# Performance work log

Hardware: AMD Instinct MI355X
Metric: run time of the kernel (lower is better)

The kernel has to match this reference:

```python
import jax, jax.numpy as jnp
import numpy as np

D_IN = 3072      # == d_out (code reshapes x directly into heads)
D_OUT = 3072
N_HEADS = 16
HEAD_DIM = D_OUT // N_HEADS          # 192
D_C = D_OUT // 3                     # 1024, compressed latent dim
LN_EPS = 1e-5


def setup_inputs() -> dict:
    key = jax.random.key(0)
    ks = jax.random.split(key, 8)
    s = 0.02
    return {
        "x": jax.random.normal(ks[0], (2, 2048, D_IN), dtype=jnp.float32),
        "W_query": jax.random.normal(ks[1], (D_OUT, D_IN), dtype=jnp.float32) * s,
        "W_kv": jax.random.normal(ks[2], (D_C, D_IN), dtype=jnp.float32) * s,
        "W_uk": jax.random.normal(ks[3], (D_OUT, D_C), dtype=jnp.float32) * s,
        "W_uv": jax.random.normal(ks[4], (D_OUT, D_C), dtype=jnp.float32) * s,
        "W_out": jax.random.normal(ks[5], (D_OUT, D_OUT), dtype=jnp.float32) * s,
        "b_out": jnp.zeros((D_OUT,), dtype=jnp.float32),
        "ln_g": jnp.ones((D_C,), dtype=jnp.float32),
        "ln_b": jnp.zeros((D_C,), dtype=jnp.float32),
    }


def reference(x, W_query, W_kv, W_uk, W_uv, W_out, b_out, ln_g, ln_b):
    B, T, D = x.shape
    past_length = 0  # prefill, kv_cache=None

    # absorbed K projection: (d_out, d_in) @ (d_out, d_c) -> (H, head_dim, d_c)
    absorbed_k = (W_query @ W_uk).reshape(N_HEADS, HEAD_DIM, D_C)

    # compressed latent c_kv = LayerNorm(x @ W_kv^T), shape (B, S, d_c)
    c = x @ W_kv.T
    mu = jnp.mean(c, axis=-1, keepdims=True)
    var = jnp.mean(jnp.square(c - mu), axis=-1, keepdims=True)
    c_kv = (c - mu) * jax.lax.rsqrt(var + LN_EPS) * ln_g + ln_b
    S = c_kv.shape[1]

    # values decompressed: (B, S, H, head_dim)
    v = (c_kv @ W_uv.T).reshape(B, S, N_HEADS, HEAD_DIM)

    # queries: raw x reshaped into heads (as in the original code)
    q = x.reshape(B, T, N_HEADS, HEAD_DIM)

    # scores in compressed space: q @ absorbed_k @ c_kv^T
    tmp = jnp.einsum("bthd,hdc->bhtc", q, absorbed_k)           # (B,H,T,d_c)
    scores = jnp.einsum("bhtc,bsc->bhts", tmp, c_kv)
    scores = scores / np.float32(np.sqrt(HEAD_DIM))

    # causal mask with past_length offset (tril diagonal=past_length)
    row = jnp.arange(T)[:, None]
    col = jnp.arange(S)[None, :]
    mask = col <= (row + past_length)                            # (T,S) bool
    scores = jnp.where(mask[None, None], scores, -jnp.inf)

    weights = jax.nn.softmax(scores, axis=-1)                    # (B,H,T,S)

    ctx = jnp.einsum("bhts,bshd->bthd", weights, v).reshape(B, T, D_OUT)
    out = ctx @ W_out.T + b_out
    return out, c_kv
```

## Files before the change

### kernel.cpp

```cpp
#include <hip/hip_runtime.h>
#include <hip/hip_bf16.h>
#include <math.h>

#define BB 2
#define TT 2048
#define DD 3072
#define NH 16
#define HD 192
#define DC 1024

typedef __attribute__((ext_vector_type(8))) short bh8;
typedef __attribute__((ext_vector_type(4))) float f32x4;
typedef unsigned int u32;

__device__ __forceinline__ short f2b(float f) {
  __hip_bfloat16 h = __float2bfloat16(f);
  return *reinterpret_cast<short*>(&h);
}

__device__ __forceinline__ void gload16(const void* g, void* lds) {
  __builtin_amdgcn_global_load_lds(
      (const __attribute__((address_space(1))) u32*)g,
      (__attribute__((address_space(3))) u32*)lds, 16, 0, 0);
}

__global__ __launch_bounds__(256) void cast_f2b_k(const float* __restrict__ in,
                                                  short* __restrict__ out) {
  size_t i = ((size_t)blockIdx.x * 256 + threadIdx.x) * 8;
  float4 v0 = *(const float4*)&in[i];
  float4 v1 = *(const float4*)&in[i + 4];
  bh8 o;
  o[0] = f2b(v0.x); o[1] = f2b(v0.y); o[2] = f2b(v0.z); o[3] = f2b(v0.w);
  o[4] = f2b(v1.x); o[5] = f2b(v1.y); o[6] = f2b(v1.z); o[7] = f2b(v1.w);
  *(bh8*)&out[i] = o;
}

__global__ __launch_bounds__(256) void castT_f2b_k(const float* __restrict__ in,
                                                   short* __restrict__ out,
                                                   int R, int C) {
  __shared__ float t[64][65];
  const int cx = blockIdx.x * 64, ry = blockIdx.y * 64;
  const int tid = threadIdx.x, lx = tid & 15, ly = tid >> 4;
#pragma unroll
  for (int i = 0; i < 4; ++i) {
    int r = ly + i * 16;
    float4 v = *(const float4*)&in[(size_t)(ry + r) * C + cx + lx * 4];
    t[r][lx * 4 + 0] = v.x; t[r][lx * 4 + 1] = v.y;
    t[r][lx * 4 + 2] = v.z; t[r][lx * 4 + 3] = v.w;
  }
  __syncthreads();
#pragma unroll
  for (int i = 0; i < 4; ++i) {
    int c = ly + i * 16;
    ushort4 v;
    v.x = (unsigned short)f2b(t[lx * 4 + 0][c]);
    v.y = (unsigned short)f2b(t[lx * 4 + 1][c]);
    v.z = (unsigned short)f2b(t[lx * 4 + 2][c]);
    v.w = (unsigned short)f2b(t[lx * 4 + 3][c]);
    *(ushort4*)&out[(size_t)(cx + c) * R + ry + lx * 4] = v;
  }
}

__global__ __launch_bounds__(256) void transpose_b16_k(
    const unsigned short* __restrict__ in, unsigned short* __restrict__ out) {
  __shared__ unsigned short t[64][65];
  const unsigned short* ib = in + (size_t)blockIdx.z * TT * DD;
  unsigned short* ob = out + (size_t)blockIdx.z * DD * TT;
  const int cx = blockIdx.x * 64, ry = blockIdx.y * 64;
  const int tid = threadIdx.x, lx = tid & 15, ly = tid >> 4;
#pragma unroll
  for (int i = 0; i < 4; ++i) {
    int r = ly + i * 16;
    ushort4 v = *(const ushort4*)&ib[(size_t)(ry + r) * DD + cx + lx * 4];
    t[r][lx * 4 + 0] = v.x; t[r][lx * 4 + 1] = v.y;
    t[r][lx * 4 + 2] = v.z; t[r][lx * 4 + 3] = v.w;
  }
  __syncthreads();
#pragma unroll
  for (int i = 0; i < 4; ++i) {
    int c = ly + i * 16;
    ushort4 v;
    v.x = t[lx * 4 + 0][c]; v.y = t[lx * 4 + 1][c];
    v.z = t[lx * 4 + 2][c]; v.w = t[lx * 4 + 3][c];
    *(ushort4*)&ob[(size_t)(cx + c) * TT + ry + lx * 4] = v;
  }
}

template <bool OUTBF, bool BIAS>
__global__ __launch_bounds__(256) void gemm_bf16(
    const short* __restrict__ A, const short* __restrict__ Bt,
    const float* __restrict__ bias, void* __restrict__ Cout,
    int M, int N, int K) {
  __shared__ short As[4096];
  __shared__ short Bs[4096];
  const int tid = threadIdx.x;
  const int w = tid >> 6, l = tid & 63, lm = l & 15, lg = l >> 4;
  const int wr = w >> 1, wc = w & 1;
  const int m0 = blockIdx.y * 128, n0 = blockIdx.x * 128;

  f32x4 acc[4][4] = {};

  for (int k0 = 0; k0 < K; k0 += 32) {
    __syncthreads();
#pragma unroll
    for (int c = 0; c < 2; ++c) {
      int p = c * 256 + w * 64 + l;
      int row = p >> 2, kc = p & 3;
      int g = kc ^ ((row >> 1) & 3);
      gload16(&A[(size_t)(m0 + row) * K + k0 + g * 8],
              &As[(c * 256 + w * 64) * 8]);
      gload16(&Bt[(size_t)(n0 + row) * K + k0 + g * 8],
              &Bs[(c * 256 + w * 64) * 8]);
    }
    __syncthreads();

    bh8 a[4], b[4];
#pragma unroll
    for (int mi = 0; mi < 4; ++mi) {
      int r = wr * 64 + mi * 16 + lm;
      a[mi] = *(const bh8*)&As[r * 32 + ((lg ^ ((r >> 1) & 3)) << 3)];
    }
#pragma unroll
    for (int ni = 0; ni < 4; ++ni) {
      int r = wc * 64 + ni * 16 + lm;
      b[ni] = *(const bh8*)&Bs[r * 32 + ((lg ^ ((r >> 1) & 3)) << 3)];
    }
#pragma unroll
    for (int mi = 0; mi < 4; ++mi)
#pragma unroll
      for (int ni = 0; ni < 4; ++ni)
        acc[mi][ni] = __builtin_amdgcn_mfma_f32_16x16x32_bf16(
            a[mi], b[ni], acc[mi][ni], 0, 0, 0);
  }

#pragma unroll
  for (int mi = 0; mi < 4; ++mi) {
#pragma unroll
    for (int ni = 0; ni < 4; ++ni) {
      int row = m0 + wr * 64 + mi * 16 + lg * 4;
      int col = n0 + wc * 64 + ni * 16 + lm;
      float bi = 0.f;
      if (BIAS) bi = bias[col];
#pragma unroll
      for (int r = 0; r < 4; ++r) {
        float v = acc[mi][ni][r] + bi;
        if (OUTBF)
          ((short*)Cout)[(size_t)(row + r) * N + col] = f2b(v);
        else
          ((float*)Cout)[(size_t)(row + r) * N + col] = v;
      }
    }
  }
}

__global__ __launch_bounds__(256) void ln_k(const float* __restrict__ cpre,
                                            const float* __restrict__ g,
                                            const float* __restrict__ bta,
                                            float* __restrict__ o32,
                                            short* __restrict__ o16) {
  const int row = blockIdx.x;
  const int tid = threadIdx.x;
  __shared__ float red1[4];
  __shared__ float red2[4];

  float4 v = *(const float4*)&cpre[(size_t)row * DC + tid * 4];
  float s = v.x + v.y + v.z + v.w;
#pragma unroll
  for (int mk = 32; mk; mk >>= 1) s += __shfl_xor(s, mk, 64);
  if ((tid & 63) == 0) red1[tid >> 6] = s;
  __syncthreads();
  float mu = (red1[0] + red1[1] + red1[2] + red1[3]) * (1.f / DC);

  float dx = v.x - mu, dy = v.y - mu, dz = v.z - mu, dw = v.w - mu;
  float s2 = dx * dx + dy * dy + dz * dz + dw * dw;
#pragma unroll
  for (int mk = 32; mk; mk >>= 1) s2 += __shfl_xor(s2, mk, 64);
  if ((tid & 63) == 0) red2[tid >> 6] = s2;
  __syncthreads();
  float var = (red2[0] + red2[1] + red2[2] + red2[3]) * (1.f / DC);
  float rs = rsqrtf(var + 1e-5f);

  float4 gg = *(const float4*)&g[tid * 4];
  float4 bb = *(const float4*)&bta[tid * 4];
  float4 o;
  o.x = dx * rs * gg.x + bb.x;
  o.y = dy * rs * gg.y + bb.y;
  o.z = dz * rs * gg.z + bb.z;
  o.w = dw * rs * gg.w + bb.w;
  *(float4*)&o32[(size_t)row * DC + tid * 4] = o;
  ushort4 ob;
  ob.x = (unsigned short)f2b(o.x); ob.y = (unsigned short)f2b(o.y);
  ob.z = (unsigned short)f2b(o.z); ob.w = (unsigned short)f2b(o.w);
  *(ushort4*)&o16[(size_t)row * DC + tid * 4] = ob;
}

__global__ __launch_bounds__(256) void attn_mfma(
    const short* __restrict__ xb, const short* __restrict__ kfull,
    const short* __restrict__ vT, short* __restrict__ ctx) {
  __shared__ short Ks[64 * 192];
  __shared__ short Vs[192 * 64];
  __shared__ short Ps[4][16 * 64];

  const int idx = blockIdx.x;
  const int qt = 31 - (idx >> 5);
  const int bh = idx & 31;
  const int h = bh & 15, b = bh >> 4;
  const int tid = threadIdx.x, w = tid >> 6, l = tid & 63;
  const int lm = l & 15, lg = l >> 4;
  const int qw0 = qt * 64 + w * 16;
  const float QS = 0.07216878364870323f;

  bh8 qf[6];
  {
    const short* qrow = &xb[(size_t)(b * TT + qw0 + lm) * DD + h * HD];
#pragma unroll
    for (int kq = 0; kq < 6; ++kq)
      qf[kq] = *(const bh8*)&qrow[kq * 32 + lg * 8];
  }

  f32x4 o[12] = {};
  float mrun[4], lrun[4];
#pragma unroll
  for (int r = 0; r < 4; ++r) { mrun[r] = -INFINITY; lrun[r] = 0.f; }

  for (int st = 0; st <= qt; ++st) {
    const int s0 = st * 64;
    __syncthreads();
#pragma unroll
    for (int c = 0; c < 6; ++c) {
      int p = c * 256 + w * 64 + l;
      {
        int krow = p / 24, kc = p - krow * 24;
        int g = kc ^ (krow & 7);
        gload16(&kfull[(size_t)(b * TT + s0 + krow) * DD + h * HD + g * 8],
                &Ks[(c * 256 + w * 64) * 8]);
      }
      {
        int vrow = p >> 3, vc = p & 7;
        int gv = vc ^ (vrow & 7);
        gload16(&vT[(size_t)((b * NH + h) * HD + vrow) * TT + s0 + gv * 8],
                &Vs[(c * 256 + w * 64) * 8]);
      }
    }
    __syncthreads();

    f32x4 s[4] = {};
    __builtin_amdgcn_s_setprio(1);
#pragma unroll
    for (int nf = 0; nf < 4; ++nf) {
      const int krow = nf * 16 + lm;
      const short* kr = &Ks[krow * 192];
#pragma unroll
      for (int kq = 0; kq < 6; ++kq) {
        bh8 kb = *(const bh8*)&kr[(((kq * 4 + lg) ^ (krow & 7)) << 3)];
        s[nf] = __builtin_amdgcn_mfma_f32_16x16x32_bf16(qf[kq], kb, s[nf],
                                                        0, 0, 0);
      }
    }
    __builtin_amdgcn_s_setprio(0);

    float pv[4][4];
#pragma unroll
    for (int nf = 0; nf < 4; ++nf)
#pragma unroll
      for (int r = 0; r < 4; ++r) pv[nf][r] = s[nf][r] * QS;
    if (st == qt) {
#pragma unroll
      for (int nf = 0; nf < 4; ++nf)
#pragma unroll
        for (int r = 0; r < 4; ++r)
          if (nf * 16 + lm > w * 16 + lg * 4 + r) pv[nf][r] = -INFINITY;
    }
#pragma unroll
    for (int r = 0; r < 4; ++r) {
      float mt = fmaxf(fmaxf(pv[0][r], pv[1][r]), fmaxf(pv[2][r], pv[3][r]));
#pragma unroll
      for (int mk = 1; mk < 16; mk <<= 1) mt = fmaxf(mt, __shfl_xor(mt, mk));
      float mnew = fmaxf(mrun[r], mt);
      float corr = __expf(mrun[r] - mnew);
      mrun[r] = mnew;
      float ls = 0.f;
#pragma unroll
      for (int nf = 0; nf < 4; ++nf) {
        float p = __expf(pv[nf][r] - mnew);
        pv[nf][r] = p;
        ls += p;
      }
#pragma unroll
      for (int mk = 1; mk < 16; mk <<= 1) ls += __shfl_xor(ls, mk);
      lrun[r] = lrun[r] * corr + ls;
#pragma unroll
      for (int nf = 0; nf < 12; ++nf) o[nf][r] *= corr;
    }
#pragma unroll
    for (int nf = 0; nf < 4; ++nf)
#pragma unroll
      for (int r = 0; r < 4; ++r) {
        int prow = lg * 4 + r;
        int col = nf * 16 + lm;
        int sc = (((col >> 3) ^ (prow & 7)) << 3) + (col & 7);
        Ps[w][prow * 64 + sc] = f2b(pv[nf][r]);
      }

    bh8 pa0, pa1;
    {
      int prow = lm;
      pa0 = *(const bh8*)&Ps[w][prow * 64 + ((lg ^ (prow & 7)) << 3)];
      pa1 = *(const bh8*)&Ps[w][prow * 64 + (((4 + lg) ^ (prow & 7)) << 3)];
    }
    __builtin_amdgcn_s_setprio(1);
#pragma unroll
    for (int nf = 0; nf < 12; ++nf) {
      int drow = nf * 16 + lm;
      const short* vr = &Vs[drow * 64];
      bh8 vb0 = *(const bh8*)&vr[((lg ^ (drow & 7)) << 3)];
      bh8 vb1 = *(const bh8*)&vr[(((4 + lg) ^ (drow & 7)) << 3)];
      o[nf] = __builtin_amdgcn_mfma_f32_16x16x32_bf16(pa0, vb0, o[nf], 0, 0, 0);
      o[nf] = __builtin_amdgcn_mfma_f32_16x16x32_bf16(pa1, vb1, o[nf], 0, 0, 0);
    }
    __builtin_amdgcn_s_setprio(0);
  }

#pragma unroll
  for (int r = 0; r < 4; ++r) {
    float inv = 1.f / lrun[r];
    int row = qw0 + lg * 4 + r;
    short* cp = &ctx[(size_t)(b * TT + row) * DD + h * HD];
#pragma unroll
    for (int nf = 0; nf < 12; ++nf)
      cp[nf * 16 + lm] = f2b(o[nf][r] * inv);
  }
}

extern "C" void kernel_launch(void* const* d_in, const int* in_sizes, int n_in,
                              void* d_out, int out_size, void* d_ws,
                              size_t ws_size, hipStream_t stream) {
  const float* x    = (const float*)d_in[0];
  const float* Wq   = (const float*)d_in[1];
  const float* Wkv  = (const float*)d_in[2];
  const float* Wuk  = (const float*)d_in[3];
  const float* Wuv  = (const float*)d_in[4];
  const float* Wout = (const float*)d_in[5];
  const float* bout = (const float*)d_in[6];
  const float* lng  = (const float*)d_in[7];
  const float* lnb  = (const float*)d_in[8];

  float* out   = (float*)d_out;
  float* ckv32 = out + (size_t)BB * TT * DD;

  char* W = (char*)d_ws;
  short* xb     = (short*)(W);
  short* wbuf   = (short*)(W + 25165824);
  short* wukT   = (short*)(W + 44040192);
  short* wkvb   = (short*)(W + 50331648);
  short* wuvb   = (short*)(W + 56623104);
  short* akb    = (short*)(W + 62914560);
  float* cpre   = (float*)(W + 69206016);
  short* ckvb   = (short*)(W + 85983232);
  short* kfullb = (short*)(W + 94371840);
  short* vfullb = (short*)(W + 119537664);
  short* vTb    = (short*)(W + 144703488);
  short* ctxb   = vfullb;

  cast_f2b_k<<<6144, 256, 0, stream>>>(x, xb);
  cast_f2b_k<<<4608, 256, 0, stream>>>(Wq, wbuf);
  cast_f2b_k<<<1536, 256, 0, stream>>>(Wkv, wkvb);
  cast_f2b_k<<<1536, 256, 0, stream>>>(Wuv, wuvb);
  castT_f2b_k<<<dim3(16, 48), 256, 0, stream>>>(Wuk, wukT, 3072, 1024);

  gemm_bf16<true, false><<<dim3(8, 24), 256, 0, stream>>>(
      wbuf, wukT, nullptr, akb, 3072, 1024, 3072);
  cast_f2b_k<<<4608, 256, 0, stream>>>(Wout, wbuf);
  gemm_bf16<false, false><<<dim3(8, 32), 256, 0, stream>>>(
      xb, wkvb, nullptr, cpre, 4096, 1024, 3072);
  ln_k<<<4096, 256, 0, stream>>>(cpre, lng, lnb, ckv32, ckvb);
  gemm_bf16<true, false><<<dim3(24, 32), 256, 0, stream>>>(
      ckvb, akb, nullptr, kfullb, 4096, 3072, 1024);
  gemm_bf16<true, false><<<dim3(24, 32), 256, 0, stream>>>(
      ckvb, wuvb, nullptr, vfullb, 4096, 3072, 1024);
  transpose_b16_k<<<dim3(48, 32, 2), 256, 0, stream>>>(
      (const unsigned short*)vfullb, (unsigned short*)vTb);
  attn_mfma<<<1024, 256, 0, stream>>>(xb, kfullb, vTb, ctxb);
  gemm_bf16<false, true><<<dim3(24, 32), 256, 0, stream>>>(
      ctxb, wbuf, bout, out, 4096, 3072, 3072);
}
```

Measured before the change: 479.6 us.

## Double-buffer attention K/V tiles, fuse K/V up-projections, lazily rescale softmax

The attention kernel now keeps two LDS buffers each for K and V. It prefetches the next 64-row tile while computing on the current one, which should hide global-load latency behind the MFMA work. The separate K and V up-projection GEMMs become one N=6144 GEMM. This relies on wuvb and akb sitting next to each other in the workspace, so the output is an interleaved [V|K] buffer with row stride 6144. The online softmax now rescales the accumulators only when the row max grows by more than 8, which skips most exp and multiply passes. The costs are roughly double the attention LDS use, which may lower occupancy, and the ctx buffer now reuses the cpre/ckvb region.

Result: slower. 565.1 us (+17.8%).

```diff
diff --git a/kernel.cpp b/kernel.cpp
--- a/kernel.cpp
+++ b/kernel.cpp
@@ -8,6 +8,7 @@
 #define NH 16
 #define HD 192
 #define DC 1024
+#define LDK 6144
 
 typedef __attribute__((ext_vector_type(8))) short bh8;
 typedef __attribute__((ext_vector_type(4))) float f32x4;
@@ -62,16 +63,17 @@
 }
 
 __global__ __launch_bounds__(256) void transpose_b16_k(
-    const unsigned short* __restrict__ in, unsigned short* __restrict__ out) {
+    const unsigned short* __restrict__ in, unsigned short* __restrict__ out,
+    int ldin) {
   __shared__ unsigned short t[64][65];
-  const unsigned short* ib = in + (size_t)blockIdx.z * TT * DD;
+  const unsigned short* ib = in + (size_t)blockIdx.z * TT * ldin;
   unsigned short* ob = out + (size_t)blockIdx.z * DD * TT;
   const int cx = blockIdx.x * 64, ry = blockIdx.y * 64;
   const int tid = threadIdx.x, lx = tid & 15, ly = tid >> 4;
 #pragma unroll
   for (int i = 0; i < 4; ++i) {
     int r = ly + i * 16;
-    ushort4 v = *(const ushort4*)&ib[(size_t)(ry + r) * DD + cx + lx * 4];
+    ushort4 v = *(const ushort4*)&ib[(size_t)(ry + r) * ldin + cx + lx * 4];
     t[r][lx * 4 + 0] = v.x; t[r][lx * 4 + 1] = v.y;
     t[r][lx * 4 + 2] = v.z; t[r][lx * 4 + 3] = v.w;
   }
@@ -195,10 +197,10 @@
 }
 
 __global__ __launch_bounds__(256) void attn_mfma(
-    const short* __restrict__ xb, const short* __restrict__ kfull,
+    const short* __restrict__ xb, const short* __restrict__ kp,
     const short* __restrict__ vT, short* __restrict__ ctx) {
-  __shared__ short Ks[64 * 192];
-  __shared__ short Vs[192 * 64];
+  __shared__ short Ks[2][64 * 192];
+  __shared__ short Vs[2][192 * 64];
   __shared__ short Ps[4][16 * 64];
 
   const int idx = blockIdx.x;
@@ -218,38 +220,44 @@
       qf[kq] = *(const bh8*)&qrow[kq * 32 + lg * 8];
   }
 
-  f32x4 o[12] = {};
-  float mrun[4], lrun[4];
-#pragma unroll
-  for (int r = 0; r < 4; ++r) { mrun[r] = -INFINITY; lrun[r] = 0.f; }
-
-  for (int st = 0; st <= qt; ++st) {
-    const int s0 = st * 64;
-    __syncthreads();
+  const int p0 = w * 64 + l;
+  auto stage = [&](int nb, int s0) {
 #pragma unroll
     for (int c = 0; c < 6; ++c) {
-      int p = c * 256 + w * 64 + l;
+      int p = c * 256 + p0;
       {
         int krow = p / 24, kc = p - krow * 24;
         int g = kc ^ (krow & 7);
-        gload16(&kfull[(size_t)(b * TT + s0 + krow) * DD + h * HD + g * 8],
-                &Ks[(c * 256 + w * 64) * 8]);
+        gload16(&kp[(size_t)(b * TT + s0 + krow) * LDK + h * HD + g * 8],
+                &Ks[nb][(c * 256 + w * 64) * 8]);
       }
       {
         int vrow = p >> 3, vc = p & 7;
         int gv = vc ^ (vrow & 7);
         gload16(&vT[(size_t)((b * NH + h) * HD + vrow) * TT + s0 + gv * 8],
-                &Vs[(c * 256 + w * 64) * 8]);
-      }
-    }
-    __syncthreads();
+                &Vs[nb][(c * 256 + w * 64) * 8]);
+      }
+    }
+  };
+
+  f32x4 o[12] = {};
+  float mrun[4], lrun[4];
+#pragma unroll
+  for (int r = 0; r < 4; ++r) { mrun[r] = -INFINITY; lrun[r] = 0.f; }
+
+  stage(0, 0);
+  __syncthreads();
+
+  for (int st = 0; st <= qt; ++st) {
+    const int cb = st & 1;
+    if (st < qt) stage(cb ^ 1, (st + 1) * 64);
 
     f32x4 s[4] = {};
     __builtin_amdgcn_s_setprio(1);
 #pragma unroll
     for (int nf = 0; nf < 4; ++nf) {
       const int krow = nf * 16 + lm;
-      const short* kr = &Ks[krow * 192];
+      const short* kr = &Ks[cb][krow * 192];
 #pragma unroll
       for (int kq = 0; kq < 6; ++kq) {
         bh8 kb = *(const bh8*)&kr[(((kq * 4 + lg) ^ (krow & 7)) << 3)];
@@ -276,21 +284,24 @@
       float mt = fmaxf(fmaxf(pv[0][r], pv[1][r]), fmaxf(pv[2][r], pv[3][r]));
 #pragma unroll
       for (int mk = 1; mk < 16; mk <<= 1) mt = fmaxf(mt, __shfl_xor(mt, mk));
-      float mnew = fmaxf(mrun[r], mt);
-      float corr = __expf(mrun[r] - mnew);
-      mrun[r] = mnew;
+      if (__any(mt > mrun[r] + 8.f)) {
+        float mnew = fmaxf(mrun[r], mt);
+        float corr = __expf(mrun[r] - mnew);
+        mrun[r] = mnew;
+        lrun[r] *= corr;
+#pragma unroll
+        for (int nf = 0; nf < 12; ++nf) o[nf][r] *= corr;
+      }
       float ls = 0.f;
 #pragma unroll
       for (int nf = 0; nf < 4; ++nf) {
-        float p = __expf(pv[nf][r] - mnew);
+        float p = __expf(pv[nf][r] - mrun[r]);
         pv[nf][r] = p;
         ls += p;
       }
 #pragma unroll
       for (int mk = 1; mk < 16; mk <<= 1) ls += __shfl_xor(ls, mk);
-      lrun[r] = lrun[r] * corr + ls;
-#pragma unroll
-      for (int nf = 0; nf < 12; ++nf) o[nf][r] *= corr;
+      lrun[r] += ls;
     }
 #pragma unroll
     for (int nf = 0; nf < 4; ++nf)
@@ -312,13 +323,15 @@
 #pragma unroll
     for (int nf = 0; nf < 12; ++nf) {
       int drow = nf * 16 + lm;
-      const short* vr = &Vs[drow * 64];
+      const short* vr = &Vs[cb][drow * 64];
       bh8 vb0 = *(const bh8*)&vr[((lg ^ (drow & 7)) << 3)];
       bh8 vb1 = *(const bh8*)&vr[(((4 + lg) ^ (drow & 7)) << 3)];
       o[nf] = __builtin_amdgcn_mfma_f32_16x16x32_bf16(pa0, vb0, o[nf], 0, 0, 0);
       o[nf] = __builtin_amdgcn_mfma_f32_16x16x32_bf16(pa1, vb1, o[nf], 0, 0, 0);
     }
     __builtin_amdgcn_s_setprio(0);
+
+    __syncthreads();
   }
 
 #pragma unroll
@@ -357,10 +370,9 @@
   short* akb    = (short*)(W + 62914560);
   float* cpre   = (float*)(W + 69206016);
   short* ckvb   = (short*)(W + 85983232);
-  short* kfullb = (short*)(W + 94371840);
-  short* vfullb = (short*)(W + 119537664);
+  short* kvbuf  = (short*)(W + 94371840);
   short* vTb    = (short*)(W + 144703488);
-  short* ctxb   = vfullb;
+  short* ctxb   = (short*)(W + 69206016);
 
   cast_f2b_k<<<6144, 256, 0, stream>>>(x, xb);
   cast_f2b_k<<<4608, 256, 0, stream>>>(Wq, wbuf);
@@ -374,13 +386,11 @@
   gemm_bf16<false, false><<<dim3(8, 32), 256, 0, stream>>>(
       xb, wkvb, nullptr, cpre, 4096, 1024, 3072);
   ln_k<<<4096, 256, 0, stream>>>(cpre, lng, lnb, ckv32, ckvb);
-  gemm_bf16<true, false><<<dim3(24, 32), 256, 0, stream>>>(
-      ckvb, akb, nullptr, kfullb, 4096, 3072, 1024);
-  gemm_bf16<true, false><<<dim3(24, 32), 256, 0, stream>>>(
-      ckvb, wuvb, nullptr, vfullb, 4096, 3072, 1024);
+  gemm_bf16<true, false><<<dim3(48, 32), 256, 0, stream>>>(
+      ckvb, wuvb, nullptr, kvbuf, 4096, 6144, 1024);
   transpose_b16_k<<<dim3(48, 32, 2), 256, 0, stream>>>(
-      (const unsigned short*)vfullb, (unsigned short*)vTb);
-  attn_mfma<<<1024, 256, 0, stream>>>(xb, kfullb, vTb, ctxb);
+      (const unsigned short*)kvbuf, (unsigned short*)vTb, LDK);
+  attn_mfma<<<1024, 256, 0, stream>>>(xb, kvbuf + 3072, vTb, ctxb);
   gemm_bf16<false, true><<<dim3(24, 32), 256, 0, stream>>>(
       ctxb, wbuf, bout, out, 4096, 3072, 3072);
 }
```

## Split-K the x@W_kv GEMM in two and remap workgroups across XCDs

Applied to the files above, without the earlier changes.

The c = x@W_kv^T GEMM (4096x1024x3072, only 256 tiles) is split along K into two halves via blockIdx.z. Each half writes its own fp32 partial buffer, and the LayerNorm kernel sums the two partials before normalizing. This is meant to fill more CUs on a low-tile-count GEMM, at the cost of an extra fp32 write and read of the partial buffer. Separately, all GEMMs now remap the flat workgroup id so consecutive tiles are spread across the 8 XCDs, aiming at better L2 locality. The second partial buffer reuses the vT workspace region, which is only written later.

Measured after the change: 469.1 us. -2.2%, faster.

```diff
diff --git a/kernel.cpp b/kernel.cpp
--- a/kernel.cpp
+++ b/kernel.cpp
@@ -62,16 +62,17 @@
 }
 
 __global__ __launch_bounds__(256) void transpose_b16_k(
-    const unsigned short* __restrict__ in, unsigned short* __restrict__ out) {
+    const unsigned short* __restrict__ in, unsigned short* __restrict__ out,
+    int ldin) {
   __shared__ unsigned short t[64][65];
-  const unsigned short* ib = in + (size_t)blockIdx.z * TT * DD;
+  const unsigned short* ib = in + (size_t)blockIdx.z * TT * ldin;
   unsigned short* ob = out + (size_t)blockIdx.z * DD * TT;
   const int cx = blockIdx.x * 64, ry = blockIdx.y * 64;
   const int tid = threadIdx.x, lx = tid & 15, ly = tid >> 4;
 #pragma unroll
   for (int i = 0; i < 4; ++i) {
     int r = ly + i * 16;
-    ushort4 v = *(const ushort4*)&ib[(size_t)(ry + r) * DD + cx + lx * 4];
+    ushort4 v = *(const ushort4*)&ib[(size_t)(ry + r) * ldin + cx + lx * 4];
     t[r][lx * 4 + 0] = v.x; t[r][lx * 4 + 1] = v.y;
     t[r][lx * 4 + 2] = v.z; t[r][lx * 4 + 3] = v.w;
   }
@@ -90,26 +91,35 @@
 __global__ __launch_bounds__(256) void gemm_bf16(
     const short* __restrict__ A, const short* __restrict__ Bt,
     const float* __restrict__ bias, void* __restrict__ Cout,
-    int M, int N, int K) {
+    int M, int N, int Klen, int lda, int ldb, size_t zoff_bytes) {
   __shared__ short As[4096];
   __shared__ short Bs[4096];
   const int tid = threadIdx.x;
   const int w = tid >> 6, l = tid & 63, lm = l & 15, lg = l >> 4;
   const int wr = w >> 1, wc = w & 1;
-  const int m0 = blockIdx.y * 128, n0 = blockIdx.x * 128;
+
+  const int bz = blockIdx.z;
+  A += (size_t)bz * Klen;
+  Bt += (size_t)bz * Klen;
+  Cout = (void*)((char*)Cout + (size_t)bz * zoff_bytes);
+
+  const int nwg = gridDim.x * gridDim.y;
+  const int flat = blockIdx.y * gridDim.x + blockIdx.x;
+  const int wgid = (flat & 7) * (nwg >> 3) + (flat >> 3);
+  const int m0 = (wgid / gridDim.x) * 128, n0 = (wgid % gridDim.x) * 128;
 
   f32x4 acc[4][4] = {};
 
-  for (int k0 = 0; k0 < K; k0 += 32) {
+  for (int k0 = 0; k0 < Klen; k0 += 32) {
     __syncthreads();
 #pragma unroll
     for (int c = 0; c < 2; ++c) {
       int p = c * 256 + w * 64 + l;
       int row = p >> 2, kc = p & 3;
       int g = kc ^ ((row >> 1) & 3);
-      gload16(&A[(size_t)(m0 + row) * K + k0 + g * 8],
+      gload16(&A[(size_t)(m0 + row) * lda + k0 + g * 8],
               &As[(c * 256 + w * 64) * 8]);
-      gload16(&Bt[(size_t)(n0 + row) * K + k0 + g * 8],
+      gload16(&Bt[(size_t)(n0 + row) * ldb + k0 + g * 8],
               &Bs[(c * 256 + w * 64) * 8]);
     }
     __syncthreads();
@@ -153,7 +163,8 @@
   }
 }
 
-__global__ __launch_bounds__(256) void ln_k(const float* __restrict__ cpre,
+__global__ __launch_bounds__(256) void ln_k(const float* __restrict__ cp0,
+                                            const float* __restrict__ cp1,
                                             const float* __restrict__ g,
                                             const float* __restrict__ bta,
                                             float* __restrict__ o32,
@@ -163,7 +174,10 @@
   __shared__ float red1[4];
   __shared__ float red2[4];
 
-  float4 v = *(const float4*)&cpre[(size_t)row * DC + tid * 4];
+  float4 va = *(const float4*)&cp0[(size_t)row * DC + tid * 4];
+  float4 vb = *(const float4*)&cp1[(size_t)row * DC + tid * 4];
+  float4 v;
+  v.x = va.x + vb.x; v.y = va.y + vb.y; v.z = va.z + vb.z; v.w = va.w + vb.w;
   float s = v.x + v.y + v.z + v.w;
 #pragma unroll
   for (int mk = 32; mk; mk >>= 1) s += __shfl_xor(s, mk, 64);
@@ -195,7 +209,7 @@
 }
 
 __global__ __launch_bounds__(256) void attn_mfma(
-    const short* __restrict__ xb, const short* __restrict__ kfull,
+    const short* __restrict__ xb, const short* __restrict__ kf,
     const short* __restrict__ vT, short* __restrict__ ctx) {
   __shared__ short Ks[64 * 192];
   __shared__ short Vs[192 * 64];
@@ -232,7 +246,7 @@
       {
         int krow = p / 24, kc = p - krow * 24;
         int g = kc ^ (krow & 7);
-        gload16(&kfull[(size_t)(b * TT + s0 + krow) * DD + h * HD + g * 8],
+        gload16(&kf[(size_t)(b * TT + s0 + krow) * DD + h * HD + g * 8],
                 &Ks[(c * 256 + w * 64) * 8]);
       }
       {
@@ -355,12 +369,14 @@
   short* wkvb   = (short*)(W + 50331648);
   short* wuvb   = (short*)(W + 56623104);
   short* akb    = (short*)(W + 62914560);
-  float* cpre   = (float*)(W + 69206016);
+  float* cpre0  = (float*)(W + 69206016);
   short* ckvb   = (short*)(W + 85983232);
   short* kfullb = (short*)(W + 94371840);
   short* vfullb = (short*)(W + 119537664);
+  float* cpre1  = (float*)(W + 144703488);
   short* vTb    = (short*)(W + 144703488);
   short* ctxb   = vfullb;
+  const size_t G2_ZOFF = (size_t)(144703488 - 69206016);
 
   cast_f2b_k<<<6144, 256, 0, stream>>>(x, xb);
   cast_f2b_k<<<4608, 256, 0, stream>>>(Wq, wbuf);
@@ -369,18 +385,18 @@
   castT_f2b_k<<<dim3(16, 48), 256, 0, stream>>>(Wuk, wukT, 3072, 1024);
 
   gemm_bf16<true, false><<<dim3(8, 24), 256, 0, stream>>>(
-      wbuf, wukT, nullptr, akb, 3072, 1024, 3072);
+      wbuf, wukT, nullptr, akb, 3072, 1024, 3072, 3072, 3072, 0);
   cast_f2b_k<<<4608, 256, 0, stream>>>(Wout, wbuf);
-  gemm_bf16<false, false><<<dim3(8, 32), 256, 0, stream>>>(
-      xb, wkvb, nullptr, cpre, 4096, 1024, 3072);
-  ln_k<<<4096, 256, 0, stream>>>(cpre, lng, lnb, ckv32, ckvb);
+  gemm_bf16<false, false><<<dim3(8, 32, 2), 256, 0, stream>>>(
+      xb, wkvb, nullptr, cpre0, 4096, 1024, 1536, 3072, 3072, G2_ZOFF);
+  ln_k<<<4096, 256, 0, stream>>>(cpre0, cpre1, lng, lnb, ckv32, ckvb);
   gemm_bf16<true, false><<<dim3(24, 32), 256, 0, stream>>>(
-      ckvb, akb, nullptr, kfullb, 4096, 3072, 1024);
+      ckvb, akb, nullptr, kfullb, 4096, 3072, 1024, 1024, 1024, 0);
   gemm_bf16<true, false><<<dim3(24, 32), 256, 0, stream>>>(
-      ckvb, wuvb, nullptr, vfullb, 4096, 3072, 1024);
+      ckvb, wuvb, nullptr, vfullb, 4096, 3072, 1024, 1024, 1024, 0);
   transpose_b16_k<<<dim3(48, 32, 2), 256, 0, stream>>>(
-      (const unsigned short*)vfullb, (unsigned short*)vTb);
+      (const unsigned short*)vfullb, (unsigned short*)vTb, DD);
   attn_mfma<<<1024, 256, 0, stream>>>(xb, kfullb, vTb, ctxb);
   gemm_bf16<false, true><<<dim3(24, 32), 256, 0, stream>>>(
-      ctxb, wbuf, bout, out, 4096, 3072, 3072);
-}
+      ctxb, wbuf, bout, out, 4096, 3072, 3072, 3072, 3072, 0);
+}
```
